# Performance work log

Hardware: AMD Instinct MI355X
Metric: run time of the kernel (lower is better)

Reference implementation:

```python
import jax, jax.numpy as jnp
import numpy as np

N = 65536      # total nodes
D = 256        # score_dim
E = 128        # embed_dim
H = 8          # num_heads
HID = 256      # MLP hidden width
G = 128        # number of graphs (segments)


def setup_inputs() -> dict:
    key = jax.random.key(0)
    ks = jax.random.split(key, 16)
    w = lambda k, shape, s=0.02: jax.random.normal(k, shape, jnp.float32) * s
    return {
        "score_matrix": jax.random.normal(ks[0], (N, D), jnp.float32),
        "x": jax.random.normal(ks[1], (N, D), jnp.float32),  # unused by forward (as in source)
        "batch": jnp.sort(jax.random.randint(ks[2], (N,), 0, G)),
        "pos": jax.random.normal(ks[3], (1, D), jnp.float32),
        "para": jax.random.normal(ks[4], (1, E), jnp.float32),
        # stacked per-head MLP weights (q, k, v): in_dim->256->embed_dim
        "Wq1": w(ks[5], (H, D, HID)), "bq1": jnp.zeros((H, HID), jnp.float32),
        "Wq2": w(ks[6], (H, HID, E)), "bq2": jnp.zeros((H, E), jnp.float32),
        "Wk1": w(ks[7], (H, D, HID)), "bk1": jnp.zeros((H, HID), jnp.float32),
        "Wk2": w(ks[8], (H, HID, E)), "bk2": jnp.zeros((H, E), jnp.float32),
        "Wv1": w(ks[9], (H, D, HID)), "bv1": jnp.zeros((H, HID), jnp.float32),
        "Wv2": w(ks[10], (H, HID, E)), "bv2": jnp.zeros((H, E), jnp.float32),
        # out MLP: (H*E)->256->E
        "Wo1": w(ks[11], (H * E, HID)), "bo1": jnp.zeros((HID,), jnp.float32),
        "Wo2": w(ks[12], (HID, E)), "bo2": jnp.zeros((E,), jnp.float32),
    }


def _head_mlp(xs, W1, b1, W2, b2):
    # xs: [N, D]; W1: [H, D, HID]; W2: [H, HID, E] -> [N, H, E]
    h = jax.nn.relu(jnp.einsum('nd,hdk->nhk', xs, W1) + b1)
    return jnp.einsum('nhk,hke->nhe', h, W2) + b2


def _segment_softmax(src, idx, num_seg):
    # grouped softmax along axis 0 (matches torch scatter_max/scatter_add version)
    m = jax.ops.segment_max(src, idx, num_segments=num_seg)
    ex = jnp.exp(src - m[idx])
    den = jax.ops.segment_sum(ex, idx, num_segments=num_seg)[idx] + 1e-16
    return ex / den


def reference(score_matrix, x, batch, pos, para,
              Wq1, bq1, Wq2, bq2, Wk1, bk1, Wk2, bk2, Wv1, bv1, Wv2, bv2,
              Wo1, bo1, Wo2, bo2):
    sm = score_matrix + pos                                  # [N, D]
    q = _head_mlp(sm, Wq1, bq1, Wq2, bq2)                    # [N, H, E]
    k = _head_mlp(sm, Wk1, bk1, Wk2, bk2)                    # [N, H, E]
    v = _head_mlp(sm, Wv1, bv1, Wv2, bv2)                    # [N, H, E]
    scores = jnp.einsum('nhe,nge->nhg', q, k) / np.float32(np.sqrt(E))  # [N, H, H]
    aw = _segment_softmax(scores, batch, G)                  # [N, H, H]
    s = jnp.einsum('nhg,nge->nhe', aw, v).reshape(sm.shape[0], H * E)   # [N, H*E]
    out = jax.nn.relu(s @ Wo1 + bo1) @ Wo2 + bo2             # [N, E]
    return out + para
```

## Files before the change

kernel.cpp:

```cpp
#include <hip/hip_runtime.h>

#define N_NODES 65536
#define NSEG    128

using s16x8 = __attribute__((ext_vector_type(8))) short;
using s16x4 = __attribute__((ext_vector_type(4))) short;
using f32x4 = __attribute__((ext_vector_type(4))) float;

__device__ __forceinline__ float bf2f(unsigned short s) {
    union { unsigned u; float f; } x; x.u = ((unsigned)s) << 16; return x.f;
}
__device__ __forceinline__ short f2bf(float f) {
    union { float f; unsigned u; } x; x.f = f;
    unsigned r = x.u + 0x7FFFu + ((x.u >> 16) & 1u);
    return (short)(r >> 16);
}
__device__ __forceinline__ void gload_lds16(const void* g, void* lds) {
    __builtin_amdgcn_global_load_lds((const __attribute__((address_space(1))) void*)g,
                                     (__attribute__((address_space(3))) void*)lds, 16, 0, 0);
}


__global__ void prep_sm_kernel(const float* __restrict__ score, const float* __restrict__ pos,
                               short* __restrict__ sm) {
    int i = blockIdx.x * blockDim.x + threadIdx.x;
    int base = i * 4;
    f32x4 s = __builtin_nontemporal_load((const f32x4*)(score + base));
    f32x4 p = *(const f32x4*)(pos + (base & 255));
    s16x4 o;
#pragma unroll
    for (int j = 0; j < 4; ++j) o[j] = f2bf(s[j] + p[j]);
    *(s16x4*)(sm + base) = o;
}

__global__ void transpose_all_kernel(const float* __restrict__ Wq1, const float* __restrict__ Wk1,
                                     const float* __restrict__ Wv1, const float* __restrict__ Wq2,
                                     const float* __restrict__ Wk2, const float* __restrict__ Wv2,
                                     const float* __restrict__ Wo1, const float* __restrict__ Wo2,
                                     short* __restrict__ W1T, short* __restrict__ W2T,
                                     short* __restrict__ Wo1T, short* __restrict__ Wo2T) {
    int t = blockIdx.x;
    const float* in; short* out; int R, C, tx, ty;
    if (t < 1536) {
        int u = t >> 6, rem = t & 63;
        const float* s = (u < 8) ? Wq1 : (u < 16) ? Wk1 : Wv1;
        in = s + (long)(u & 7) * 65536; out = W1T + (long)u * 65536;
        R = 256; C = 256; tx = rem & 7; ty = rem >> 3;
    } else if (t < 2304) {
        int t2 = t - 1536, u = t2 >> 5, rem = t2 & 31;
        const float* s = (u < 8) ? Wq2 : (u < 16) ? Wk2 : Wv2;
        in = s + (long)(u & 7) * 32768; out = W2T + (long)u * 32768;
        R = 256; C = 128; tx = rem & 3; ty = rem >> 2;
    } else if (t < 2560) {
        int t3 = t - 2304;
        in = Wo1; out = Wo1T; R = 1024; C = 256; tx = t3 & 7; ty = t3 >> 3;
    } else {
        int t4 = t - 2560;
        in = Wo2; out = Wo2T; R = 256; C = 128; tx = t4 & 3; ty = t4 >> 2;
    }
    __shared__ float tbuf[32][33];
    const int c0 = tx * 32, r0 = ty * 32;
    const int lx = threadIdx.x & 31, ly = threadIdx.x >> 5;
#pragma unroll
    for (int i = 0; i < 32; i += 8)
        tbuf[ly + i][lx] = in[(long)(r0 + ly + i) * C + c0 + lx];
    __syncthreads();
#pragma unroll
    for (int i = 0; i < 32; i += 8)
        out[(long)(c0 + ly + i) * R + r0 + lx] = f2bf(tbuf[lx][ly + i]);
}

__global__ void prep_small_kernel(const float* __restrict__ bq1, const float* __restrict__ bk1,
                                  const float* __restrict__ bv1, const float* __restrict__ bq2,
                                  const float* __restrict__ bk2, const float* __restrict__ bv2,
                                  const float* __restrict__ bo2, const float* __restrict__ para,
                                  float* __restrict__ b1cat, float* __restrict__ b2cat,
                                  float* __restrict__ bo2p) {
    int i = blockIdx.x * blockDim.x + threadIdx.x;
    if (i < 6144) {
        int u = i >> 8, j = i & 255;
        const float* s = (u < 8) ? (bq1 + u * 256 + j)
                       : (u < 16) ? (bk1 + (u - 8) * 256 + j)
                                  : (bv1 + (u - 16) * 256 + j);
        b1cat[i] = *s;
    } else if (i < 9216) {
        int ii = i - 6144;
        int u = ii >> 7, j = ii & 127;
        const float* s = (u < 8) ? (bq2 + u * 128 + j)
                       : (u < 16) ? (bk2 + (u - 8) * 128 + j)
                                  : (bv2 + (u - 16) * 128 + j);
        b2cat[ii] = *s;
    } else if (i < 9344) {
        int e = i - 9216;
        bo2p[e] = bo2[e] + para[e];
    }
}


template <bool OUTBF16>
__global__ __launch_bounds__(512, 2)
void fused_mlp(const short* __restrict__ A, int lda,
               const short* __restrict__ B1, long b1_ustride,
               const float* __restrict__ bias1, int bias1_ustride,
               const short* __restrict__ B2, long b2_ustride,
               const float* __restrict__ bias2, int bias2_ustride,
               void* __restrict__ Cv, int ldc, long c_ustride, int K1) {
    const int u = blockIdx.y;
    B1    += (long)u * b1_ustride;
    bias1 += (long)u * bias1_ustride;
    B2    += (long)u * b2_ustride;
    bias2 += (long)u * bias2_ustride;

    __shared__ __align__(16) short lds[24576];
    short* Bs = lds;
    short* As = lds + 8192;
    short* hs = lds + 8192;

    const int tid = threadIdx.x, lane = tid & 63, wave = tid >> 6;
    const int wm = wave >> 2;
    const int wn = wave & 3;
    const int brow = blockIdx.x * 128;

    const int lrow = lane >> 3;
    const int schk = ((lane & 7) ^ lrow) * 8;
    const int nkt1 = K1 >> 6;
    const int l15 = lane & 15, lq = lane >> 4;

    f32x4 acc2[4][2];
#pragma unroll
    for (int i = 0; i < 4; ++i)
#pragma unroll
        for (int j = 0; j < 2; ++j) acc2[i][j] = (f32x4){0.f, 0.f, 0.f, 0.f};

    for (int p = 0; p < 2; ++p) {
        f32x4 acc1[4][2];
#pragma unroll
        for (int i = 0; i < 4; ++i)
#pragma unroll
            for (int j = 0; j < 2; ++j) acc1[i][j] = (f32x4){0.f, 0.f, 0.f, 0.f};

        for (int kt = 0; kt < nkt1; ++kt) {
            __syncthreads();
            const int ko = kt * 64;
#pragma unroll
            for (int i = 0; i < 2; ++i) {
                int cch = wave * 2 + i;
                int r = cch * 8 + lrow;
                gload_lds16(A  + (long)(brow + r) * lda + ko + schk, &As[cch * 512]);
                gload_lds16(B1 + (long)(p * 128 + r) * K1 + ko + schk, &Bs[cch * 512]);
            }
            __syncthreads();
#pragma unroll
            for (int kk = 0; kk < 2; ++kk) {
                const int slot = (((kk * 4) + lq) ^ (lane & 7)) * 8;
                s16x8 af[4], bfv[2];
#pragma unroll
                for (int i = 0; i < 4; ++i)
                    af[i] = *(const s16x8*)&As[(wm * 64 + i * 16 + l15) * 64 + slot];
#pragma unroll
                for (int j = 0; j < 2; ++j)
                    bfv[j] = *(const s16x8*)&Bs[(wn * 32 + j * 16 + l15) * 64 + slot];
#pragma unroll
                for (int i = 0; i < 4; ++i)
#pragma unroll
                    for (int j = 0; j < 2; ++j)
                        acc1[i][j] = __builtin_amdgcn_mfma_f32_16x16x32_bf16(bfv[j], af[i], acc1[i][j], 0, 0, 0);
            }
        }

        __syncthreads();

#pragma unroll
        for (int i = 0; i < 2; ++i) {
            int cch = wave * 2 + i;
            int r = cch * 8 + lrow;
            gload_lds16(B2 + (long)r * 256 + p * 128 + schk, &Bs[cch * 512]);
        }

        {
            const int cbq = lq << 2;
#pragma unroll
            for (int j = 0; j < 2; ++j) {
                int cb = wn * 32 + j * 16 + cbq;
                f32x4 bv = *(const f32x4*)(bias1 + p * 128 + cb);
#pragma unroll
                for (int i = 0; i < 4; ++i) {
                    int node = wm * 64 + i * 16 + l15;
                    s16x4 hv;
#pragma unroll
                    for (int r = 0; r < 4; ++r)
                        hv[r] = f2bf(fmaxf(acc1[i][j][r] + bv[r], 0.f));
                    *(s16x4*)&hs[node * 128 + (((cb >> 3) ^ (node & 7)) << 3) + (cb & 7)] = hv;
                }
            }
        }

#pragma unroll
        for (int kt2 = 0; kt2 < 2; ++kt2) {
            __syncthreads();
#pragma unroll
            for (int kk = 0; kk < 2; ++kk) {
                const int slotb = (((kk * 4) + lq) ^ (lane & 7)) * 8;
                s16x8 hf[4], wf[2];
#pragma unroll
                for (int i = 0; i < 4; ++i) {
                    int row = wm * 64 + i * 16 + l15;
                    int c = kt2 * 8 + kk * 4 + lq;
                    hf[i] = *(const s16x8*)&hs[row * 128 + ((c ^ (row & 7)) << 3)];
                }
#pragma unroll
                for (int j = 0; j < 2; ++j)
                    wf[j] = *(const s16x8*)&Bs[(wn * 32 + j * 16 + l15) * 64 + slotb];
#pragma unroll
                for (int i = 0; i < 4; ++i)
#pragma unroll
                    for (int j = 0; j < 2; ++j)
                        acc2[i][j] = __builtin_amdgcn_mfma_f32_16x16x32_bf16(wf[j], hf[i], acc2[i][j], 0, 0, 0);
            }
            if (kt2 == 0) {
                __syncthreads();
#pragma unroll
                for (int i = 0; i < 2; ++i) {
                    int cch = wave * 2 + i;
                    int r = cch * 8 + lrow;
                    gload_lds16(B2 + (long)r * 256 + p * 128 + 64 + schk, &Bs[cch * 512]);
                }
            }
        }
    }

    const int cbq = lq << 2;
    if (OUTBF16) {
        __syncthreads();
        short* Cs = hs;
#pragma unroll
        for (int j = 0; j < 2; ++j) {
            int cb = wn * 32 + j * 16 + cbq;
            f32x4 bv = *(const f32x4*)(bias2 + cb);
#pragma unroll
            for (int i = 0; i < 4; ++i) {
                int node = wm * 64 + i * 16 + l15;
                s16x4 ov;
#pragma unroll
                for (int r = 0; r < 4; ++r) ov[r] = f2bf(acc2[i][j][r] + bv[r]);
                *(s16x4*)&Cs[node * 128 + (((cb >> 3) ^ (node & 7)) << 3) + (cb & 7)] = ov;
            }
        }
        __syncthreads();
        short* cbase = (short*)Cv + u * c_ustride + (long)brow * ldc;
#pragma unroll
        for (int p8 = 0; p8 < 4; ++p8) {
            int g = tid + p8 * 512;
            int row = g >> 4, ck = g & 15;
            s16x8 val = *(const s16x8*)&Cs[row * 128 + ((ck ^ (row & 7)) * 8)];
            *(s16x8*)(cbase + (long)row * ldc + ck * 8) = val;
        }
    } else {
        float* cbase = (float*)Cv + u * c_ustride;
#pragma unroll
        for (int j = 0; j < 2; ++j) {
            int cb = wn * 32 + j * 16 + cbq;
            f32x4 bv = *(const f32x4*)(bias2 + cb);
#pragma unroll
            for (int i = 0; i < 4; ++i) {
                int node = wm * 64 + i * 16 + l15;
                f32x4 o;
#pragma unroll
                for (int r = 0; r < 4; ++r) o[r] = acc2[i][j][r] + bv[r];
                *(f32x4*)&cbase[(long)(brow + node) * ldc + cb] = o;
            }
        }
    }
}


__global__ void scores_mfma_kernel(const short* __restrict__ qk, float* __restrict__ scores,
                                   int nc) {
    const int lane = threadIdx.x & 63;
    int gw = (blockIdx.x * blockDim.x + threadIdx.x) >> 6;
    int nw = (gridDim.x * blockDim.x) >> 6;
    const int npairs = nc >> 1;
    const int r = lane & 15, ks = lane >> 4;
    for (int p = gw; p < npairs; p += nw) {
        const long n0 = (long)p * 2;
        const short* qp = qk + (n0 + (r >> 3)) * 2048 + (r & 7) * 128 + ks * 8;
        const short* kp = qp + 1024;
        f32x4 acc = (f32x4){0.f, 0.f, 0.f, 0.f};
#pragma unroll
        for (int kt = 0; kt < 4; ++kt) {
            s16x8 a = *(const s16x8*)(qp + kt * 32);
            s16x8 b = *(const s16x8*)(kp + kt * 32);
            acc = __builtin_amdgcn_mfma_f32_16x16x32_bf16(a, b, acc, 0, 0, 0);
        }
        const int c = lane & 15, rr0 = (lane >> 4) * 4;
        if ((rr0 >> 3) == (c >> 3)) {
            float* o = scores + (n0 + (rr0 >> 3)) * 64 + (c & 7);
#pragma unroll
            for (int reg = 0; reg < 4; ++reg)
                o[((rr0 & 7) + reg) * 8] = acc[reg] * 0.08838834764831845f;
        }
    }
}

__global__ void segstats1_kernel(const float* __restrict__ scores, const int* __restrict__ batch,
                                 float* __restrict__ pm, float* __restrict__ ps) {
    const int g = blockIdx.x, sl = blockIdx.y;
    int lo = 0, hi = N_NODES;
    while (lo < hi) { int mid = (lo + hi) >> 1; if (batch[mid] < g) lo = mid + 1; else hi = mid; }
    const int start = lo;
    hi = N_NODES;
    while (lo < hi) { int mid = (lo + hi) >> 1; if (batch[mid] <= g) lo = mid + 1; else hi = mid; }
    const int end = lo;
    const int len = end - start;
    const int s0 = start + (len * sl) / 8;
    const int s1 = start + (len * (sl + 1)) / 8;

    const int e = threadIdx.x & 63, sub = threadIdx.x >> 6;
    __shared__ float red[4][64];
    float m = -1e30f;
    for (int n = s0 + sub; n < s1; n += 4)
        m = fmaxf(m, scores[(long)n * 64 + e]);
    red[sub][e] = m;
    __syncthreads();
    m = fmaxf(fmaxf(red[0][e], red[1][e]), fmaxf(red[2][e], red[3][e]));
    __syncthreads();
    float s = 0.f;
    for (int n = s0 + sub; n < s1; n += 4)
        s += expf(scores[(long)n * 64 + e] - m);
    red[sub][e] = s;
    __syncthreads();
    if (sub == 0) {
        int idx = (g * 8 + sl) * 64 + e;
        pm[idx] = m;
        ps[idx] = red[0][e] + red[1][e] + red[2][e] + red[3][e];
    }
}

__global__ void segstats2_kernel(const float* __restrict__ pm, const float* __restrict__ ps,
                                 float* __restrict__ segm, float* __restrict__ segdinv) {
    const int g = blockIdx.x, e = threadIdx.x;
    float M = -1e30f;
#pragma unroll
    for (int sl = 0; sl < 8; ++sl)
        M = fmaxf(M, pm[(g * 8 + sl) * 64 + e]);
    float den = 1e-16f;
#pragma unroll
    for (int sl = 0; sl < 8; ++sl) {
        int idx = (g * 8 + sl) * 64 + e;
        den += ps[idx] * expf(pm[idx] - M);
    }
    segm[g * 64 + e]    = M;
    segdinv[g * 64 + e] = 1.f / den;
}

__global__ void pv_kernel(const short* __restrict__ v, short* __restrict__ sout,
                          const float* __restrict__ scores, const int* __restrict__ batch,
                          const float* __restrict__ segm, const float* __restrict__ segdinv,
                          int n0) {
    __shared__ float aw[16][64];
    const int t = threadIdx.x;
    const int nodeL0 = blockIdx.x * 16;
    {
        int j0 = t * 4;
        int nl = j0 >> 6, e0 = j0 & 63;
        int n = n0 + nodeL0 + nl;
        int b = batch[n];
        f32x4 sc = *(const f32x4*)(scores + (long)n * 64 + e0);
#pragma unroll
        for (int i = 0; i < 4; ++i)
            aw[nl][e0 + i] = expf(sc[i] - segm[b * 64 + e0 + i]) * segdinv[b * 64 + e0 + i];
    }
    __syncthreads();
    const int nl = t >> 4;
    const int ec = (t & 15) * 8;
    const long nloc = nodeL0 + nl;
    const short* vp = v + nloc * 1024 + ec;
    float acc[8][8];
#pragma unroll
    for (int h = 0; h < 8; ++h)
#pragma unroll
        for (int j = 0; j < 8; ++j) acc[h][j] = 0.f;
#pragma unroll
    for (int g = 0; g < 8; ++g) {
        s16x8 vv = *(const s16x8*)(vp + g * 128);
        float vf[8];
#pragma unroll
        for (int j = 0; j < 8; ++j) vf[j] = bf2f((unsigned short)vv[j]);
#pragma unroll
        for (int h = 0; h < 8; ++h) {
            float wgt = aw[nl][h * 8 + g];
#pragma unroll
            for (int j = 0; j < 8; ++j) acc[h][j] += wgt * vf[j];
        }
    }
#pragma unroll
    for (int h = 0; h < 8; ++h) {
        s16x8 o;
#pragma unroll
        for (int j = 0; j < 8; ++j) o[j] = f2bf(acc[h][j]);
        *(s16x8*)(sout + nloc * 1024 + h * 128 + ec) = o;
    }
}


extern "C" void kernel_launch(void* const* d_in, const int* in_sizes, int n_in,
                              void* d_out, int out_size, void* d_ws, size_t ws_size,
                              hipStream_t stream) {
    const float* score = (const float*)d_in[0];
    const int*   batch = (const int*)d_in[2];
    const float* pos   = (const float*)d_in[3];
    const float* para  = (const float*)d_in[4];
    const float* Wq1 = (const float*)d_in[5];
    const float* bq1 = (const float*)d_in[6];
    const float* Wq2 = (const float*)d_in[7];
    const float* bq2 = (const float*)d_in[8];
    const float* Wk1 = (const float*)d_in[9];
    const float* bk1 = (const float*)d_in[10];
    const float* Wk2 = (const float*)d_in[11];
    const float* bk2 = (const float*)d_in[12];
    const float* Wv1 = (const float*)d_in[13];
    const float* bv1 = (const float*)d_in[14];
    const float* Wv2 = (const float*)d_in[15];
    const float* bv2 = (const float*)d_in[16];
    const float* Wo1 = (const float*)d_in[17];
    const float* bo1 = (const float*)d_in[18];
    const float* Wo2 = (const float*)d_in[19];
    const float* bo2 = (const float*)d_in[20];
    float* out = (float*)d_out;
    (void)in_sizes; (void)n_in; (void)out_size;

    char* w = (char*)d_ws;
    short* sm     = (short*)w; w += (size_t)N_NODES * 256 * 2;
    float* scoresb= (float*)w; w += (size_t)N_NODES * 64 * 4;
    short* W1T    = (short*)w; w += (size_t)24 * 256 * 256 * 2;
    short* W2T    = (short*)w; w += (size_t)24 * 128 * 256 * 2;
    short* Wo1T   = (short*)w; w += (size_t)256 * 1024 * 2;
    short* Wo2T   = (short*)w; w += (size_t)128 * 256 * 2;
    float* b1cat  = (float*)w; w += 6144 * 4;
    float* b2cat  = (float*)w; w += 3072 * 4;
    float* bo2p   = (float*)w; w += 1024;
    float* segm   = (float*)w; w += 8192 * 4;
    float* segdi  = (float*)w; w += 8192 * 4;
    float* pm     = (float*)w; w += 65536 * 4;
    float* ps     = (float*)w; w += 65536 * 4;
    size_t persist = (size_t)(w - (char*)d_ws);
    size_t area = ws_size - persist;

    int NC = 32768;
    while (NC > 1024 && (size_t)NC * 4096 > area) NC >>= 1;
    const int nchunks = N_NODES / NC;
    short* X = (short*)w;

    prep_sm_kernel<<<N_NODES * 256 / 4 / 256, 256, 0, stream>>>(score, pos, sm);
    transpose_all_kernel<<<2592, 256, 0, stream>>>(Wq1, Wk1, Wv1, Wq2, Wk2, Wv2, Wo1, Wo2,
                                                   W1T, W2T, Wo1T, Wo2T);
    prep_small_kernel<<<37, 256, 0, stream>>>(bq1, bk1, bv1, bq2, bk2, bv2, bo2, para,
                                              b1cat, b2cat, bo2p);

    for (int c = 0; c < nchunks; ++c) {
        const int n0 = c * NC;
        fused_mlp<true><<<dim3(NC / 128, 16), 512, 0, stream>>>(
            sm + (size_t)n0 * 256, 256, W1T, 65536, b1cat, 256,
            W2T, 32768, b2cat, 128, X, 2048, 128, 256);
        scores_mfma_kernel<<<NC / 8, 256, 0, stream>>>(X, scoresb + (size_t)n0 * 64, NC);
    }

    segstats1_kernel<<<dim3(NSEG, 8), 256, 0, stream>>>(scoresb, batch, pm, ps);
    segstats2_kernel<<<NSEG, 64, 0, stream>>>(pm, ps, segm, segdi);

    const size_t sfull_bytes = (size_t)N_NODES * 2048;
    if (area >= sfull_bytes + (size_t)4096 * 2048) {
        int NCB = 16384;
        while ((size_t)NCB * 2048 + sfull_bytes > area) NCB >>= 1;
        short* sfull = (short*)w;
        short* v     = sfull + (size_t)N_NODES * 1024;
        for (int c = 0; c < N_NODES / NCB; ++c) {
            const int n0 = c * NCB;
            fused_mlp<true><<<dim3(NCB / 128, 8), 512, 0, stream>>>(
                sm + (size_t)n0 * 256, 256, W1T + 16 * 65536, 65536, b1cat + 16 * 256, 256,
                W2T + 16 * 32768, 32768, b2cat + 16 * 128, 128, v, 1024, 128, 256);
            pv_kernel<<<NCB / 16, 256, 0, stream>>>(v, sfull + (size_t)n0 * 1024,
                                                    scoresb, batch, segm, segdi, n0);
        }
        fused_mlp<false><<<dim3(N_NODES / 128, 1), 512, 0, stream>>>(
            sfull, 1024, Wo1T, 0, bo1, 0, Wo2T, 0, bo2p, 0, out, 128, 0, 1024);
    } else {
        int NCB = 32768;
        while (NCB > 1024 && (size_t)NCB * 4096 > area) NCB >>= 1;
        short* v = (short*)w;
        short* s = v + (size_t)NCB * 1024;
        for (int c = 0; c < N_NODES / NCB; ++c) {
            const int n0 = c * NCB;
            fused_mlp<true><<<dim3(NCB / 128, 8), 512, 0, stream>>>(
                sm + (size_t)n0 * 256, 256, W1T + 16 * 65536, 65536, b1cat + 16 * 256, 256,
                W2T + 16 * 32768, 32768, b2cat + 16 * 128, 128, v, 1024, 128, 256);
            pv_kernel<<<NCB / 16, 256, 0, stream>>>(v, s, scoresb, batch, segm, segdi, n0);
            fused_mlp<false><<<dim3(NCB / 128, 1), 512, 0, stream>>>(
                s, 1024, Wo1T, 0, bo1, 0, Wo2T, 0, bo2p, 0,
                out + (size_t)n0 * 128, 128, 0, 1024);
        }
    }
}
```

Before: 603.8 us.

## Double-buffer LDS in fused MLP to overlap global loads with MFMA

Grows shared memory from 48KB to 64KB and splits it into four regions so the next K tile of A and B1 is staged via global_load_lds while the current tile feeds MFMAs. The second-layer W2 tiles are prefetched into free regions during the tail of the first GEMM, which removes a barrier and a serialized load in the second GEMM. The cost is more LDS per block, which can lower occupancy under the 512-thread launch bounds of 2 blocks, and the loop now assumes an even number of K tiles.

Result: slower. 733.0 us (+21.4%).

```diff
diff --git a/kernel.cpp b/kernel.cpp
--- a/kernel.cpp
+++ b/kernel.cpp
@@ -111,10 +111,12 @@
     B2    += (long)u * b2_ustride;
     bias2 += (long)u * bias2_ustride;
 
-    __shared__ __align__(16) short lds[24576];
-    short* Bs = lds;
-    short* As = lds + 8192;
-    short* hs = lds + 8192;
+    __shared__ __align__(16) short lds[32768];
+    short* R0 = lds;
+    short* R1 = lds + 8192;
+    short* R2 = lds + 16384;
+    short* R3 = lds + 24576;
+    short* hs = R2;
 
     const int tid = threadIdx.x, lane = tid & 63, wave = tid >> 6;
     const int wm = wave >> 2;
@@ -126,56 +128,68 @@
     const int nkt1 = K1 >> 6;
     const int l15 = lane & 15, lq = lane >> 4;
 
+    const int cch0 = wave * 2, cch1 = wave * 2 + 1;
+    const int ar0 = cch0 * 8 + lrow, ar1 = cch1 * 8 + lrow;
+
     f32x4 acc2[4][2];
 #pragma unroll
     for (int i = 0; i < 4; ++i)
 #pragma unroll
         for (int j = 0; j < 2; ++j) acc2[i][j] = (f32x4){0.f, 0.f, 0.f, 0.f};
 
+#define STAGE_AB(kt, RA, RB)                                                        \
+    {                                                                               \
+        const int ko = (kt) * 64;                                                   \
+        gload_lds16(A + (long)(brow + ar0) * lda + ko + schk, &(RA)[cch0 * 512]);   \
+        gload_lds16(A + (long)(brow + ar1) * lda + ko + schk, &(RA)[cch1 * 512]);   \
+        gload_lds16(B1 + (long)(p * 128 + ar0) * K1 + ko + schk, &(RB)[cch0 * 512]);\
+        gload_lds16(B1 + (long)(p * 128 + ar1) * K1 + ko + schk, &(RB)[cch1 * 512]);\
+    }
+#define STAGE_W2(t, RW)                                                             \
+    {                                                                               \
+        gload_lds16(B2 + (long)ar0 * 256 + p * 128 + (t) * 64 + schk, &(RW)[cch0 * 512]); \
+        gload_lds16(B2 + (long)ar1 * 256 + p * 128 + (t) * 64 + schk, &(RW)[cch1 * 512]); \
+    }
+#define MFMA_G1(RA, RB)                                                             \
+    _Pragma("unroll")                                                               \
+    for (int kk = 0; kk < 2; ++kk) {                                                \
+        const int slot = (((kk * 4) + lq) ^ (lane & 7)) * 8;                        \
+        s16x8 af[4], bfv[2];                                                        \
+        _Pragma("unroll")                                                           \
+        for (int i = 0; i < 4; ++i)                                                 \
+            af[i] = *(const s16x8*)&(RA)[(wm * 64 + i * 16 + l15) * 64 + slot];     \
+        _Pragma("unroll")                                                           \
+        for (int j = 0; j < 2; ++j)                                                 \
+            bfv[j] = *(const s16x8*)&(RB)[(wn * 32 + j * 16 + l15) * 64 + slot];    \
+        _Pragma("unroll")                                                           \
+        for (int i = 0; i < 4; ++i)                                                 \
+            _Pragma("unroll")                                                       \
+            for (int j = 0; j < 2; ++j)                                             \
+                acc1[i][j] = __builtin_amdgcn_mfma_f32_16x16x32_bf16(bfv[j], af[i], acc1[i][j], 0, 0, 0); \
+    }
+
     for (int p = 0; p < 2; ++p) {
+        STAGE_AB(0, R0, R1);
+
         f32x4 acc1[4][2];
 #pragma unroll
         for (int i = 0; i < 4; ++i)
 #pragma unroll
             for (int j = 0; j < 2; ++j) acc1[i][j] = (f32x4){0.f, 0.f, 0.f, 0.f};
 
-        for (int kt = 0; kt < nkt1; ++kt) {
+        for (int kt = 0; kt < nkt1; kt += 2) {
             __syncthreads();
-            const int ko = kt * 64;
-#pragma unroll
-            for (int i = 0; i < 2; ++i) {
-                int cch = wave * 2 + i;
-                int r = cch * 8 + lrow;
-                gload_lds16(A  + (long)(brow + r) * lda + ko + schk, &As[cch * 512]);
-                gload_lds16(B1 + (long)(p * 128 + r) * K1 + ko + schk, &Bs[cch * 512]);
-            }
+            STAGE_AB(kt + 1, R2, R3);
+            MFMA_G1(R0, R1);
             __syncthreads();
-#pragma unroll
-            for (int kk = 0; kk < 2; ++kk) {
-                const int slot = (((kk * 4) + lq) ^ (lane & 7)) * 8;
-                s16x8 af[4], bfv[2];
-#pragma unroll
-                for (int i = 0; i < 4; ++i)
-                    af[i] = *(const s16x8*)&As[(wm * 64 + i * 16 + l15) * 64 + slot];
-#pragma unroll
-                for (int j = 0; j < 2; ++j)
-                    bfv[j] = *(const s16x8*)&Bs[(wn * 32 + j * 16 + l15) * 64 + slot];
-#pragma unroll
-                for (int i = 0; i < 4; ++i)
-#pragma unroll
-                    for (int j = 0; j < 2; ++j)
-                        acc1[i][j] = __builtin_amdgcn_mfma_f32_16x16x32_bf16(bfv[j], af[i], acc1[i][j], 0, 0, 0);
-            }
+            if (kt + 2 < nkt1) { STAGE_AB(kt + 2, R0, R1); }
+            else               { STAGE_W2(0, R0); }
+            MFMA_G1(R2, R3);
         }
 
         __syncthreads();
 
-#pragma unroll
-        for (int i = 0; i < 2; ++i) {
-            int cch = wave * 2 + i;
-            int r = cch * 8 + lrow;
-            gload_lds16(B2 + (long)r * 256 + p * 128 + schk, &Bs[cch * 512]);
-        }
+        STAGE_W2(1, R1);
 
         {
             const int cbq = lq << 2;
@@ -195,9 +209,11 @@
             }
         }
 
-#pragma unroll
-        for (int kt2 = 0; kt2 < 2; ++kt2) {
-            __syncthreads();
+        __syncthreads();
+
+#pragma unroll
+        for (int half = 0; half < 2; ++half) {
+            const short* RW = half ? R1 : R0;
 #pragma unroll
             for (int kk = 0; kk < 2; ++kk) {
                 const int slotb = (((kk * 4) + lq) ^ (lane & 7)) * 8;
@@ -205,34 +221,29 @@
 #pragma unroll
                 for (int i = 0; i < 4; ++i) {
                     int row = wm * 64 + i * 16 + l15;
-                    int c = kt2 * 8 + kk * 4 + lq;
+                    int c = half * 8 + kk * 4 + lq;
                     hf[i] = *(const s16x8*)&hs[row * 128 + ((c ^ (row & 7)) << 3)];
                 }
 #pragma unroll
                 for (int j = 0; j < 2; ++j)
-                    wf[j] = *(const s16x8*)&Bs[(wn * 32 + j * 16 + l15) * 64 + slotb];
+                    wf[j] = *(const s16x8*)&RW[(wn * 32 + j * 16 + l15) * 64 + slotb];
 #pragma unroll
                 for (int i = 0; i < 4; ++i)
 #pragma unroll
                     for (int j = 0; j < 2; ++j)
                         acc2[i][j] = __builtin_amdgcn_mfma_f32_16x16x32_bf16(wf[j], hf[i], acc2[i][j], 0, 0, 0);
             }
-            if (kt2 == 0) {
-                __syncthreads();
-#pragma unroll
-                for (int i = 0; i < 2; ++i) {
-                    int cch = wave * 2 + i;
-                    int r = cch * 8 + lrow;
-                    gload_lds16(B2 + (long)r * 256 + p * 128 + 64 + schk, &Bs[cch * 512]);
-                }
-            }
-        }
-    }
+        }
+
+        __syncthreads();
+    }
+#undef STAGE_AB
+#undef STAGE_W2
+#undef MFMA_G1
 
     const int cbq = lq << 2;
     if (OUTBF16) {
-        __syncthreads();
-        short* Cs = hs;
+        short* Cs = R0;
 #pragma unroll
         for (int j = 0; j < 2; ++j) {
             int cb = wn * 32 + j * 16 + cbq;
```
